# Optimization experiments

Measured on AMD Instinct MI355X. Metric: run time of the kernel, lower is better.

## Reference

```python
import jax, jax.numpy as jnp
import numpy as np

N_EMBD = 1024
HEAD_SIZE = 64
BATCH = 4
T = 4096  # == block_size


def setup_inputs() -> dict:
    key = jax.random.key(0)
    kx, kq, kk, kv = jax.random.split(key, 4)
    x = jax.random.normal(kx, (BATCH, T, N_EMBD), dtype=jnp.float32)
    Wq = jax.random.normal(kq, (N_EMBD, HEAD_SIZE), dtype=jnp.float32) * 0.02
    Wk = jax.random.normal(kk, (N_EMBD, HEAD_SIZE), dtype=jnp.float32) * 0.02
    Wv = jax.random.normal(kv, (N_EMBD, HEAD_SIZE), dtype=jnp.float32) * 0.02
    return {"x": x, "Wq": Wq, "Wk": Wk, "Wv": Wv}


def reference(x, Wq, Wk, Wv):
    # x: [B, T, C]; projections: [B, T, H]
    B, Tlen, C = x.shape
    q = jnp.einsum('btc,ch->bth', x, Wq)
    k = jnp.einsum('btc,ch->bth', x, Wk)
    v = jnp.einsum('btc,ch->bth', x, Wv)
    # NOTE: original scales by C**-0.5 where C = n_embd (input channels), not head_size
    scale = jnp.asarray(C, x.dtype) ** -0.5
    wei = jnp.einsum('bth,bsh->bts', q, k) * scale  # [B, T, T]
    causal = jnp.tril(jnp.ones((Tlen, Tlen), dtype=bool))
    wei = jnp.where(causal, wei, -jnp.inf)
    wei = jax.nn.softmax(wei, axis=-1)
    # dropout p=0.0 -> identity
    out = jnp.einsum('bts,bsh->bth', wei, v)  # [B, T, H]
    return out
```

## Files before the change

kernel.cpp:

```cpp
#include <hip/hip_runtime.h>
#include <math.h>

#define T_SEQ 4096
#define NBATCH 4
#define NEMBD 1024
#define HS 64
#define BT (NBATCH * T_SEQ)

typedef float f32x4 __attribute__((ext_vector_type(4)));
typedef short s8v  __attribute__((ext_vector_type(8)));
typedef short s4v  __attribute__((ext_vector_type(4)));

__device__ __forceinline__ short f2b_rne(float f) {
    union { float f; unsigned u; } v; v.f = f;
    unsigned r = v.u + 0x7fffu + ((v.u >> 16) & 1u);
    return (short)(r >> 16);
}
__device__ __forceinline__ unsigned pk2(float lo, float hi) {
    return __builtin_amdgcn_perm(__float_as_uint(hi), __float_as_uint(lo), 0x07060302u);
}

__global__ __launch_bounds__(256) void xcast_kernel(
        const float* __restrict__ x, short* __restrict__ xb) {
    size_t i = ((size_t)blockIdx.x * 256 + threadIdx.x) * 16;
    float4 a = *(const float4*)(x + i);
    float4 b = *(const float4*)(x + i + 4);
    float4 c = *(const float4*)(x + i + 8);
    float4 d = *(const float4*)(x + i + 12);
    union { s8v v; unsigned u[4]; } v0, v1;
    v0.u[0] = pk2(a.x, a.y); v0.u[1] = pk2(a.z, a.w);
    v0.u[2] = pk2(b.x, b.y); v0.u[3] = pk2(b.z, b.w);
    v1.u[0] = pk2(c.x, c.y); v1.u[1] = pk2(c.z, c.w);
    v1.u[2] = pk2(d.x, d.y); v1.u[3] = pk2(d.z, d.w);
    *(s8v*)(xb + i) = v0.v;
    *(s8v*)(xb + i + 8) = v1.v;
}

__global__ __launch_bounds__(256) void xtouch_kernel(
        const float* __restrict__ x, float* __restrict__ sink) {
    const float4* p = (const float4*)x;
    float s = 0.f;
    #pragma unroll
    for (int it = 0; it < 8; it++) {
        float4 v = p[(size_t)blockIdx.x * 2048 + it * 256 + threadIdx.x];
        s += v.x + v.y + v.z + v.w;
    }
    if (s == 1.0e38f) sink[0] = s;
}

__global__ __launch_bounds__(256) void wtrans_kernel(
        const float* __restrict__ Wq, const float* __restrict__ Wk,
        const float* __restrict__ Wv, short* __restrict__ Wt) {
    int e = blockIdx.x * 256 + threadIdx.x;
    int col = e & 63, k = (e >> 6) & 1023, mat = e >> 16;
    const float* W = (mat == 0) ? Wq : ((mat == 1) ? Wk : Wv);
    float scale = (mat == 0) ? 0.0450842298f : 1.0f;
    Wt[(size_t)(mat * 64 + col) * 1024 + k] = f2b_rne(W[k * 64 + col] * scale);
}

template<bool SRC_BF16>
__global__ __launch_bounds__(512) void proj_kernel(
        const void* __restrict__ xsrc, const short* __restrict__ Wt,
        short* __restrict__ QKV) {
    __shared__ short xs[32 * 72];
    __shared__ short wsh[192 * 72];
    int tid = threadIdx.x;
    int w = tid >> 6, l = tid & 63, quad = l >> 4, c16 = l & 15;
    int rt = w >> 2, cg = w & 3;
    int row0 = blockIdx.x * 32;
    short* VpT = QKV + 2 * (size_t)BT * HS;

    const short* xb = (const short*)xsrc;
    const float* xf = (const float*)xsrc;
    int xrow_b = tid >> 3,  xc8 = (tid & 7) * 8;
    int xrow_f = tid >> 4,  xc4 = (tid & 15) * 4;

    s8v  wreg[3];
    s8v  xreg_b;
    float4 xreg_f;
    #pragma unroll
    for (int i = 0; i < 3; i++) {
        int c = tid + 512 * i;
        wreg[i] = *(const s8v*)(Wt + (size_t)(c >> 3) * 1024 + ((c & 7) * 8));
    }
    if (SRC_BF16) {
        if (tid < 256) xreg_b = *(const s8v*)(xb + (size_t)(row0 + xrow_b) * 1024 + xc8);
    } else {
        xreg_f = *(const float4*)(xf + (size_t)(row0 + xrow_f) * 1024 + xc4);
    }

    f32x4 acc[3] = {};
    for (int ko = 0; ko < NEMBD; ko += 64) {
        #pragma unroll
        for (int i = 0; i < 3; i++) {
            int c = tid + 512 * i;
            *(s8v*)(wsh + (c >> 3) * 72 + ((c & 7) * 8)) = wreg[i];
        }
        if (SRC_BF16) {
            if (tid < 256) *(s8v*)(xs + xrow_b * 72 + xc8) = xreg_b;
        } else {
            union { s4v v; unsigned u[2]; } pkv;
            pkv.u[0] = pk2(xreg_f.x, xreg_f.y);
            pkv.u[1] = pk2(xreg_f.z, xreg_f.w);
            *(s4v*)(xs + xrow_f * 72 + xc4) = pkv.v;
        }
        __syncthreads();
        {
            int kn = (ko + 64 < NEMBD) ? (ko + 64) : 0;
            #pragma unroll
            for (int i = 0; i < 3; i++) {
                int c = tid + 512 * i;
                wreg[i] = *(const s8v*)(Wt + (size_t)(c >> 3) * 1024 + kn + ((c & 7) * 8));
            }
            if (SRC_BF16) {
                if (tid < 256) xreg_b = *(const s8v*)(xb + (size_t)(row0 + xrow_b) * 1024 + kn + xc8);
            } else {
                xreg_f = *(const float4*)(xf + (size_t)(row0 + xrow_f) * 1024 + kn + xc4);
            }
        }
        #pragma unroll
        for (int ks = 0; ks < 2; ks++) {
            s8v a = *(const s8v*)(xs + (rt * 16 + c16) * 72 + ks * 32 + quad * 8);
            #pragma unroll
            for (int j = 0; j < 3; j++) {
                s8v b = *(const s8v*)(wsh + (cg * 48 + j * 16 + c16) * 72 + ks * 32 + quad * 8);
                acc[j] = __builtin_amdgcn_mfma_f32_16x16x32_bf16(a, b, acc[j], 0, 0, 0);
            }
        }
        __syncthreads();
    }
    #pragma unroll
    for (int j = 0; j < 3; j++) {
        int g = cg * 48 + j * 16 + c16;
        int mat = g >> 6, h = g & 63;
        if (mat < 2) {
            #pragma unroll
            for (int r = 0; r < 4; r++) {
                int row = row0 + rt * 16 + quad * 4 + r;
                QKV[(size_t)mat * BT * HS + (size_t)row * HS + h] = f2b_rne(acc[j][r]);
            }
        } else {
            int tg = row0 + rt * 16 + quad * 4;
            int b = tg >> 12, t = tg & 4095;
            size_t base = (((size_t)((b * 64 + (t >> 6)) * 64 + h)) << 6) + (t & 63);
            s4v pv;
            #pragma unroll
            for (int r = 0; r < 4; r++) pv[r] = f2b_rne(acc[j][r]);
            *(s4v*)(VpT + base) = pv;
        }
    }
}

__global__ __launch_bounds__(512, 4) void attn_kernel(
        const short* __restrict__ QKV, float* __restrict__ out) {
    __shared__ float smem[9216];
    short* Ps = (short*)smem;

    int tid = threadIdx.x;
    int w = tid >> 6, l = tid & 63, quad = l >> 4, c16 = l & 15;
    int bi = blockIdx.x;
    int b  = bi & 3;
    int jt = 127 - (bi >> 2);
    int q0 = jt * 32;

    const short* Qp  = QKV;
    const short* Kp  = QKV + (size_t)BT * HS;
    const short* VpT = QKV + 2 * (size_t)BT * HS;
    size_t bT = (size_t)b * T_SEQ;

    s8v qf[2][2];
    #pragma unroll
    for (int qt = 0; qt < 2; qt++)
        #pragma unroll
        for (int h = 0; h < 2; h++)
            qf[qt][h] = *(const s8v*)(Qp + (bT + q0 + qt * 16 + c16) * HS + h * 32 + quad * 8);

    f32x4 o[2][4] = {};
    float lsum[2] = {0.f, 0.f};
    int nkt = (q0 >> 6) + 1;
    short* Pw[2] = { Ps + (w * 2) * 1152, Ps + (w * 2 + 1) * 1152 };
    const short* kbase = Kp + (bT + c16) * HS + quad * 8;
    const short* vbase = VpT + (((size_t)((b * 64) * 64 + c16)) << 6) + quad * 8;

    for (int kt = w; kt < nkt; kt += 8) {
        int kb = kt * 64;
        bool last = (kt == nkt - 1);

        s8v kf[4][2];
        #pragma unroll
        for (int nt = 0; nt < 4; nt++) {
            const short* kr = kbase + (size_t)(kb + nt * 16) * HS;
            kf[nt][0] = *(const s8v*)kr;
            kf[nt][1] = *(const s8v*)(kr + 32);
        }
        f32x4 st[2][4];
        #pragma unroll
        for (int nt = 0; nt < 4; nt++) {
            f32x4 z0 = {0.f, 0.f, 0.f, 0.f}, z1 = {0.f, 0.f, 0.f, 0.f};
            z0 = __builtin_amdgcn_mfma_f32_16x16x32_bf16(kf[nt][0], qf[0][0], z0, 0, 0, 0);
            z0 = __builtin_amdgcn_mfma_f32_16x16x32_bf16(kf[nt][1], qf[0][1], z0, 0, 0, 0);
            z1 = __builtin_amdgcn_mfma_f32_16x16x32_bf16(kf[nt][0], qf[1][0], z1, 0, 0, 0);
            z1 = __builtin_amdgcn_mfma_f32_16x16x32_bf16(kf[nt][1], qf[1][1], z1, 0, 0, 0);
            st[0][nt] = z0; st[1][nt] = z1;
        }
        s8v vf[4][2];
        #pragma unroll
        for (int nt = 0; nt < 4; nt++) {
            const short* vr = vbase + (((size_t)(kt * 64 + nt * 16)) << 6);
            vf[nt][0] = *(const s8v*)vr;
            vf[nt][1] = *(const s8v*)(vr + 32);
        }
        #pragma unroll
        for (int qt = 0; qt < 2; qt++) {
            int qrow = q0 + qt * 16 + c16;
            #pragma unroll
            for (int nt = 0; nt < 4; nt++) {
                float p[4];
                #pragma unroll
                for (int r = 0; r < 4; r++) {
                    float v = st[qt][nt][r];
                    if (last && (kb + nt * 16 + quad * 4 + r > qrow)) v = -30000.f;
                    p[r] = __builtin_amdgcn_exp2f(v);
                    lsum[qt] += p[r];
                }
                union { s4v v; unsigned u[2]; } pkv;
                pkv.u[0] = pk2(p[0], p[1]); pkv.u[1] = pk2(p[2], p[3]);
                *(s4v*)(Pw[qt] + c16 * 72 + nt * 16 + quad * 4) = pkv.v;
            }
        }
        s8v pa[2][2];
        #pragma unroll
        for (int qt = 0; qt < 2; qt++) {
            pa[qt][0] = *(const s8v*)(Pw[qt] + c16 * 72 + quad * 8);
            pa[qt][1] = *(const s8v*)(Pw[qt] + c16 * 72 + quad * 8 + 32);
        }
        #pragma unroll
        for (int nt = 0; nt < 4; nt++)
            #pragma unroll
            for (int qt = 0; qt < 2; qt++) {
                o[qt][nt] = __builtin_amdgcn_mfma_f32_16x16x32_bf16(pa[qt][0], vf[nt][0], o[qt][nt], 0, 0, 0);
                o[qt][nt] = __builtin_amdgcn_mfma_f32_16x16x32_bf16(pa[qt][1], vf[nt][1], o[qt][nt], 0, 0, 0);
            }
    }

    #pragma unroll
    for (int qt = 0; qt < 2; qt++) {
        lsum[qt] += __shfl_xor(lsum[qt], 16);
        lsum[qt] += __shfl_xor(lsum[qt], 32);
    }

    #pragma unroll
    for (int qt = 0; qt < 2; qt++) {
        __syncthreads();
        #pragma unroll
        for (int nt = 0; nt < 4; nt++)
            *(f32x4*)(smem + ((w * 4 + nt) * 64 + l) * 4) = o[qt][nt];
        if (l < 16) smem[8192 + w * 16 + l] = lsum[qt];
        __syncthreads();
        if (w < 4) {
            f32x4 os = {0.f, 0.f, 0.f, 0.f}, ls = {0.f, 0.f, 0.f, 0.f};
            #pragma unroll
            for (int s = 0; s < 8; s++) {
                os += *(const f32x4*)(smem + ((s * 4 + w) * 64 + l) * 4);
                ls += *(const f32x4*)(smem + 8192 + s * 16 + quad * 4);
            }
            #pragma unroll
            for (int r = 0; r < 4; r++)
                out[(bT + q0 + qt * 16 + quad * 4 + r) * HS + w * 16 + c16] = os[r] / ls[r];
        }
    }
}

extern "C" void kernel_launch(void* const* d_in, const int* in_sizes, int n_in,
                              void* d_out, int out_size, void* d_ws, size_t ws_size,
                              hipStream_t stream) {
    const float* x  = (const float*)d_in[0];
    const float* Wq = (const float*)d_in[1];
    const float* Wk = (const float*)d_in[2];
    const float* Wv = (const float*)d_in[3];
    float* out = (float*)d_out;

    short* QKV = (short*)d_ws;
    short* Wt  = QKV + (size_t)3 * BT * HS;
    short* xb  = Wt + (size_t)192 * 1024;
    size_t need = ((size_t)3 * BT * HS + (size_t)192 * 1024 + (size_t)BT * NEMBD) * 2;

    wtrans_kernel<<<768, 256, 0, stream>>>(Wq, Wk, Wv, Wt);
    if (ws_size >= need) {
        xcast_kernel<<<4096, 256, 0, stream>>>(x, xb);
        proj_kernel<true><<<BT / 32, 512, 0, stream>>>(xb, Wt, QKV);
    } else {
        xtouch_kernel<<<2048, 256, 0, stream>>>(x, (float*)d_ws);
        proj_kernel<false><<<BT / 32, 512, 0, stream>>>(x, Wt, QKV);
    }
    attn_kernel<<<512, 512, 0, stream>>>(QKV, out);
}
```

Measured before the change: 169.2 us.

## Prefetch next K tile in registers and interleave heavy/light query blocks

Loads the K fragments for the next iteration (kt+8) during the current iteration, after the V loads, so the global K load latency overlaps with softmax and PV MFMA work. It also remaps block indices so heavy (late) and light (early) causal query tiles are scheduled in an interleaved order across batches, aiming at better load balance across CUs. This raises register pressure from holding prefetched K alongside V and scores, which could lower occupancy under the 512x4 launch bounds.

After: 205.2 us. 1.21x slower.

```diff
diff --git a/kernel.cpp b/kernel.cpp
--- a/kernel.cpp
+++ b/kernel.cpp
@@ -159,8 +159,10 @@
     int tid = threadIdx.x;
     int w = tid >> 6, l = tid & 63, quad = l >> 4, c16 = l & 15;
     int bi = blockIdx.x;
-    int b  = bi & 3;
-    int jt = 127 - (bi >> 2);
+    int b  = (bi & 7) >> 1;
+    int r8 = bi >> 3;
+    int p  = bi & 1;
+    int jt = (r8 < 32) ? (127 - (2 * r8 + p)) : (2 * (r8 - 32) + p);
     int q0 = jt * 32;
 
     const short* Qp  = QKV;
@@ -182,17 +184,20 @@
     const short* kbase = Kp + (bT + c16) * HS + quad * 8;
     const short* vbase = VpT + (((size_t)((b * 64) * 64 + c16)) << 6) + quad * 8;
 
+    s8v kf[4][2];
+    if (w < nkt) {
+        #pragma unroll
+        for (int nt = 0; nt < 4; nt++) {
+            const short* kr = kbase + (size_t)(w * 64 + nt * 16) * HS;
+            kf[nt][0] = *(const s8v*)kr;
+            kf[nt][1] = *(const s8v*)(kr + 32);
+        }
+    }
+
     for (int kt = w; kt < nkt; kt += 8) {
         int kb = kt * 64;
         bool last = (kt == nkt - 1);
 
-        s8v kf[4][2];
-        #pragma unroll
-        for (int nt = 0; nt < 4; nt++) {
-            const short* kr = kbase + (size_t)(kb + nt * 16) * HS;
-            kf[nt][0] = *(const s8v*)kr;
-            kf[nt][1] = *(const s8v*)(kr + 32);
-        }
         f32x4 st[2][4];
         #pragma unroll
         for (int nt = 0; nt < 4; nt++) {
@@ -210,21 +215,29 @@
             vf[nt][0] = *(const s8v*)vr;
             vf[nt][1] = *(const s8v*)(vr + 32);
         }
+        if (kt + 8 < nkt) {
+            #pragma unroll
+            for (int nt = 0; nt < 4; nt++) {
+                const short* kr = kbase + (size_t)((kt + 8) * 64 + nt * 16) * HS;
+                kf[nt][0] = *(const s8v*)kr;
+                kf[nt][1] = *(const s8v*)(kr + 32);
+            }
+        }
         #pragma unroll
         for (int qt = 0; qt < 2; qt++) {
             int qrow = q0 + qt * 16 + c16;
             #pragma unroll
             for (int nt = 0; nt < 4; nt++) {
-                float p[4];
+                float pr[4];
                 #pragma unroll
-                for (int r = 0; r < 4; r++) {
-                    float v = st[qt][nt][r];
-                    if (last && (kb + nt * 16 + quad * 4 + r > qrow)) v = -30000.f;
-                    p[r] = __builtin_amdgcn_exp2f(v);
-                    lsum[qt] += p[r];
+                for (int rr = 0; rr < 4; rr++) {
+                    float v = st[qt][nt][rr];
+                    if (last && (kb + nt * 16 + quad * 4 + rr > qrow)) v = -30000.f;
+                    pr[rr] = __builtin_amdgcn_exp2f(v);
+                    lsum[qt] += pr[rr];
                 }
                 union { s4v v; unsigned u[2]; } pkv;
-                pkv.u[0] = pk2(p[0], p[1]); pkv.u[1] = pk2(p[2], p[3]);
+                pkv.u[0] = pk2(pr[0], pr[1]); pkv.u[1] = pk2(pr[2], pr[3]);
                 *(s4v*)(Pw[qt] + c16 * 72 + nt * 16 + quad * 4) = pkv.v;
             }
         }
@@ -265,8 +278,8 @@
                 ls += *(const f32x4*)(smem + 8192 + s * 16 + quad * 4);
             }
             #pragma unroll
-            for (int r = 0; r < 4; r++)
-                out[(bT + q0 + qt * 16 + quad * 4 + r) * HS + w * 16 + c16] = os[r] / ls[r];
+            for (int rr = 0; rr < 4; rr++)
+                out[(bT + q0 + qt * 16 + quad * 4 + rr) * HS + w * 16 + c16] = os[rr] / ls[rr];
         }
     }
 }
```
